# Kernel tuning notes

Hardware: AMD Instinct MI355X
Metric: run time of the kernel (lower is better)

The kernel has to match this reference:

```python
import jax, jax.numpy as jnp
import numpy as np

KERNEL = 25  # hard-coded moving-average kernel in the torch Model
HID = 128


def moving_avg(x):
    # x: [B, L, C]; edge-pad (KERNEL-1)//2 on each side along time, then mean over window
    p = (KERNEL - 1) // 2
    front = jnp.repeat(x[:, 0:1, :], p, axis=1)
    end = jnp.repeat(x[:, -1:, :], p, axis=1)
    xp = jnp.concatenate([front, x, end], axis=1)  # [B, L+2p, C]
    cs = jnp.cumsum(xp, axis=1)
    cs = jnp.concatenate([jnp.zeros_like(cs[:, :1, :]), cs], axis=1)
    return (cs[:, KERNEL:, :] - cs[:, :-KERNEL, :]) / KERNEL  # [B, L, C]


def memory_enhance(repres, memory):
    # repres: [N, 128], memory: [F, 128]
    attention = jax.nn.softmax(jnp.einsum('nd,fd->nf', repres, memory), axis=1)
    output = jnp.einsum('nf,fd->nd', attention, memory)
    return jnp.concatenate([output, repres], axis=1)  # [N, 256]


def setup_inputs() -> dict:
    key = jax.random.key(0)
    ks = jax.random.split(key, 12)
    B, L, C, P, M = 128, 720, 321, 336, 512
    s = lambda k, shape, fan: jax.random.normal(k, shape, jnp.float32) * (1.0 / np.sqrt(fan))
    return {
        'x': jax.random.normal(ks[0], (B, L, C), jnp.float32),
        'W_s1': s(ks[1], (HID, L), L), 'b_s1': jnp.zeros((HID,), jnp.float32),
        'W_s2': s(ks[2], (P, 2 * HID), 2 * HID), 'b_s2': jnp.zeros((P,), jnp.float32),
        'W_t1': s(ks[3], (HID, L), L), 'b_t1': jnp.zeros((HID,), jnp.float32),
        'W_t2': s(ks[4], (P, 2 * HID), 2 * HID), 'b_t2': jnp.zeros((P,), jnp.float32),
        'mem_S': s(ks[5], (M, HID), HID),
        'mem_T': s(ks[6], (M, HID), HID),
    }


def reference(x, W_s1, b_s1, W_s2, b_s2, W_t1, b_t1, W_t2, b_t2, mem_S, mem_T):
    B, L, C = x.shape
    trend = moving_avg(x)                 # [B, L, C]
    seasonal = x - trend
    seasonal = jnp.transpose(seasonal, (0, 2, 1))  # [B, C, L]
    trend = jnp.transpose(trend, (0, 2, 1))

    def branch(init, W1, b1, mem, W2, b2):
        r = jax.nn.sigmoid(jnp.einsum('bcl,hl->bch', init, W1) + b1)  # [B, C, 128]
        r = r.reshape(-1, HID)
        r = memory_enhance(r, mem)                                    # [N, 256]
        r = r.reshape(B, C, 2 * HID)
        return jnp.einsum('bcd,pd->bcp', r, W2) + b2                  # [B, C, P]

    seasonal_out = branch(seasonal, W_s1, b_s1, mem_S, W_s2, b_s2)
    trend_out = branch(trend, W_t1, b_t1, mem_T, W_t2, b_t2)
    return jnp.transpose(seasonal_out + trend_out, (0, 2, 1))  # [B, P, C]
```

## Files before the change

kernel.cpp:

```cpp
#include <hip/hip_runtime.h>
#include <math.h>

#define BB 128
#define LL 720
#define CC 321
#define HH 128
#define PP 336
#define MM 512
#define LPAD 736

typedef __attribute__((ext_vector_type(8))) short bf16x8;
typedef __attribute__((ext_vector_type(4))) float f32x4;

__device__ __forceinline__ short f2bf(float x) {
  unsigned u = __builtin_bit_cast(unsigned, x);
  u = (u + 0x7FFFu + ((u >> 16) & 1u)) >> 16;
  return (short)u;
}

__device__ __forceinline__ int packpos(int kw) {
  return ((kw & 15) >> 2) * 8 + (kw >> 4) * 4 + (kw & 3);
}

__global__ void weff_kernel(const float* __restrict__ Ws1,
                            const float* __restrict__ Wt1,
                            short* __restrict__ WsT,
                            short* __restrict__ WtT) {
  int idx = blockIdx.x * 256 + threadIdx.x;
  if (idx >= HH * LPAD) return;
  int j = idx % LPAD, h = idx / LPAD;
  int t = j >> 5, kw = j & 31;
  int dst = h * LPAD + t * 32 + packpos(kw);
  if (j >= LL) { WsT[dst] = 0; WtT[dst] = 0; return; }
  float ss = 0.f, st = 0.f;
  if (j == 0) {
    for (int l = 0; l <= 12; ++l) {
      float w = 13.f - (float)l;
      ss += w * Ws1[h * LL + l];
      st += w * Wt1[h * LL + l];
    }
  } else if (j == LL - 1) {
    for (int d = 0; d <= 12; ++d) {
      float w = 13.f - (float)d;
      ss += w * Ws1[h * LL + LL - 1 - d];
      st += w * Wt1[h * LL + LL - 1 - d];
    }
  } else {
    int lo = j - 12 < 0 ? 0 : j - 12;
    int hi = j + 12 > LL - 1 ? LL - 1 : j + 12;
    for (int l = lo; l <= hi; ++l) {
      ss += Ws1[h * LL + l];
      st += Wt1[h * LL + l];
    }
  }
  ss *= (1.f / 25.f);
  st *= (1.f / 25.f);
  WsT[dst] = f2bf(Ws1[h * LL + j] - ss);
  WtT[dst] = f2bf(st);
}

__global__ void memstage_kernel(const float* __restrict__ memS,
                                const float* __restrict__ memT,
                                short* __restrict__ stgS,
                                short* __restrict__ stgT) {
  int e = blockIdx.x * 256 + threadIdx.x;
  int br = e >> 14;
  int s = e & 16383;
  const float* src = br ? memT : memS;
  short* dst = br ? stgT : stgS;
  int tt = s >> 11;
  int c = s & 2047;
  int row = c >> 4, slot = c & 15;
  int sp = slot ^ (row & 7);
  int k = sp >> 2, lg = sp & 3;
  int ft = tt >> 1;
  short out[8];
  if ((tt & 1) == 0) {
    const float* r0 = src + (size_t)(ft * 128 + row) * 128 + k * 32 + lg * 4;
#pragma unroll
    for (int j = 0; j < 4; ++j) {
      out[j] = f2bf(r0[j]);
      out[j + 4] = f2bf(r0[16 + j]);
    }
  } else {
    int fbase = ft * 128 + k * 32 + lg * 4;
#pragma unroll
    for (int j = 0; j < 4; ++j) {
      out[j] = f2bf(src[(size_t)(fbase + j) * 128 + row]);
      out[j + 4] = f2bf(src[(size_t)(fbase + 16 + j) * 128 + row]);
    }
  }
  short4 a = make_short4(out[0], out[1], out[2], out[3]);
  short4 b = make_short4(out[4], out[5], out[6], out[7]);
  *(short4*)&dst[(size_t)s * 8] = a;
  *(short4*)&dst[(size_t)s * 8 + 4] = b;
}

__global__ void w2cvt_kernel(const float* __restrict__ Ws2,
                             const float* __restrict__ Wt2,
                             const float* __restrict__ bs2,
                             const float* __restrict__ bt2,
                             short* __restrict__ W2b, float* __restrict__ b2) {
  int i = blockIdx.x * 256 + threadIdx.x;
  if (i < PP) b2[i] = bs2[i] + bt2[i];
  if (i >= PP * 512) return;
  int p = i >> 9, k = i & 511;
  float v = (k < 256) ? Ws2[p * 256 + k] : Wt2[p * 256 + (k - 256)];
  W2b[p * 512 + (k >> 5) * 32 + packpos(k & 31)] = f2bf(v);
}

__global__ __launch_bounds__(256) void gemm1_mfma(
    const float* __restrict__ x,
    const short* __restrict__ WsT, const short* __restrict__ WtT,
    const float* __restrict__ bs1, const float* __restrict__ bt1,
    short* __restrict__ r2s, short* __restrict__ r2t) {
  __shared__ __align__(16) short wlds[2][2][128 * 40];
  __shared__ __align__(16) short xlds[2][64 * 40];
  int tid = threadIdx.x;
  int w = tid >> 6, l = tid & 63, lr = l & 15, lg = l >> 4;
  int ngrp = w >> 1, hhalf = w & 1, hb = hhalf * 64;
  int nb = blockIdx.x * 64;
  int cc0 = ngrp * 32 + lr, cc1 = cc0 + 16;
  int n0 = nb + cc0, n1 = nb + cc1;

  int rowA = tid >> 2, q = tid & 3;
  int rowB = rowA + 64;
  const short* gSA = WsT + rowA * LPAD + q * 8;
  const short* gSB = WsT + rowB * LPAD + q * 8;
  const short* gTA = WtT + rowA * LPAD + q * 8;
  const short* gTB = WtT + rowB * LPAD + q * 8;
  int dA = rowA * 40 + q * 8, dB = rowB * 40 + q * 8;

  int xcc = tid & 63, kg = tid >> 6;
  int xn = nb + xcc;
  int xb_ = xn / CC, xc_ = xn - xb_ * CC;
  const float* xptr = x + (size_t)xb_ * (LL * CC) + xc_;
  int dx0 = xcc * 40 + ((kg & 1) * 2 + 0) * 8 + (kg >> 1) * 4;
  int dx1 = xcc * 40 + ((kg & 1) * 2 + 1) * 8 + (kg >> 1) * 4;

  f32x4 acc[2][4][2];
#pragma unroll
  for (int br = 0; br < 2; ++br)
#pragma unroll
    for (int i = 0; i < 4; ++i)
#pragma unroll
      for (int rt = 0; rt < 2; ++rt) acc[br][i][rt] = (f32x4){0.f, 0.f, 0.f, 0.f};

  {
    int4 sA = *(const int4*)gSA;
    int4 sB = *(const int4*)gSB;
    int4 tA = *(const int4*)gTA;
    int4 tB = *(const int4*)gTB;
    *(int4*)&wlds[0][0][dA] = sA;
    *(int4*)&wlds[0][0][dB] = sB;
    *(int4*)&wlds[0][1][dA] = tA;
    *(int4*)&wlds[0][1][dB] = tB;
    float xf[8];
#pragma unroll
    for (int j = 0; j < 8; ++j) {
      int k = kg * 8 + j;
      xf[j] = xptr[(size_t)k * CC];
    }
    short4 s0 = make_short4(f2bf(xf[0]), f2bf(xf[1]), f2bf(xf[2]), f2bf(xf[3]));
    short4 s1 = make_short4(f2bf(xf[4]), f2bf(xf[5]), f2bf(xf[6]), f2bf(xf[7]));
    *(short4*)&xlds[0][dx0] = s0;
    *(short4*)&xlds[0][dx1] = s1;
  }
  __syncthreads();

  int cur = 0;
  for (int step = 0; step < 23; ++step) {
    int4 nSA = {0, 0, 0, 0}, nSB = nSA, nTA = nSA, nTB = nSA;
    float xf[8] = {0.f};
    if (step < 22) {
      int ko = (step + 1) * 32;
      nSA = *(const int4*)(gSA + ko);
      nSB = *(const int4*)(gSB + ko);
      nTA = *(const int4*)(gTA + ko);
      nTB = *(const int4*)(gTB + ko);
#pragma unroll
      for (int j = 0; j < 8; ++j) {
        int k = ko + kg * 8 + j;
        xf[j] = (k < LL) ? xptr[(size_t)k * CC] : 0.f;
      }
    }

    const short* xl = &xlds[cur][0];
    bf16x8 bx0 = *(const bf16x8*)&xl[cc0 * 40 + lg * 8];
    bf16x8 bx1 = *(const bf16x8*)&xl[cc1 * 40 + lg * 8];
    const short* tS = &wlds[cur][0][0];
    const short* tT = &wlds[cur][1][0];
#pragma unroll
    for (int ht = 0; ht < 4; ++ht) {
      int h = hb + ht * 16 + lr;
      bf16x8 aS = *(const bf16x8*)&tS[h * 40 + lg * 8];
      bf16x8 aT = *(const bf16x8*)&tT[h * 40 + lg * 8];
      acc[0][ht][0] =
          __builtin_amdgcn_mfma_f32_16x16x32_bf16(aS, bx0, acc[0][ht][0], 0, 0, 0);
      acc[0][ht][1] =
          __builtin_amdgcn_mfma_f32_16x16x32_bf16(aS, bx1, acc[0][ht][1], 0, 0, 0);
      acc[1][ht][0] =
          __builtin_amdgcn_mfma_f32_16x16x32_bf16(aT, bx0, acc[1][ht][0], 0, 0, 0);
      acc[1][ht][1] =
          __builtin_amdgcn_mfma_f32_16x16x32_bf16(aT, bx1, acc[1][ht][1], 0, 0, 0);
    }

    if (step < 22) {
      short* bS = &wlds[cur ^ 1][0][0];
      short* bT = &wlds[cur ^ 1][1][0];
      *(int4*)&bS[dA] = nSA;
      *(int4*)&bS[dB] = nSB;
      *(int4*)&bT[dA] = nTA;
      *(int4*)&bT[dB] = nTB;
      short4 s0 = make_short4(f2bf(xf[0]), f2bf(xf[1]), f2bf(xf[2]), f2bf(xf[3]));
      short4 s1 = make_short4(f2bf(xf[4]), f2bf(xf[5]), f2bf(xf[6]), f2bf(xf[7]));
      *(short4*)&xlds[cur ^ 1][dx0] = s0;
      *(short4*)&xlds[cur ^ 1][dx1] = s1;
    }
    __syncthreads();
    cur ^= 1;
  }

#pragma unroll
  for (int rt = 0; rt < 2; ++rt) {
    int n = rt ? n1 : n0;
    short* rowS = r2s + (size_t)n * 256 + 128;
    short* rowT = r2t + (size_t)n * 256 + 128;
#pragma unroll
    for (int ht = 0; ht < 4; ++ht) {
      int h = hb + ht * 16 + lg * 4;
      int hbase = hb + ht * 16;
      int dst = (hbase >> 5) * 32 + lg * 8 + ((hbase >> 4) & 1) * 4;
      float4 bS = *(const float4*)&bs1[h];
      float4 bT = *(const float4*)&bt1[h];
      const float* pbS = &bS.x;
      const float* pbT = &bT.x;
      short4 ss, st;
      short* ps = &ss.x;
      short* pt = &st.x;
#pragma unroll
      for (int j = 0; j < 4; ++j) {
        ps[j] = f2bf(1.f / (1.f + __expf(-(acc[0][ht][rt][j] + pbS[j]))));
        pt[j] = f2bf(1.f / (1.f + __expf(-(acc[1][ht][rt][j] + pbT[j]))));
      }
      *(short4*)&rowS[dst] = ss;
      *(short4*)&rowT[dst] = st;
    }
  }
}

__global__ __launch_bounds__(256) void memenh_mfma(
    const short* __restrict__ stgS, const short* __restrict__ stgT,
    short* __restrict__ r2s, short* __restrict__ r2t) {
  int br = blockIdx.y;
  const short* stg = br ? stgT : stgS;
  short* r2 = br ? r2t : r2s;

  __shared__ __align__(16) short buf[2][16384];
  int tid = threadIdx.x;
  int l = tid & 63, lr = l & 15, lg = l >> 4;
  int wbase = tid & 192;
  int n = blockIdx.x * 64 + (tid >> 6) * 16 + lr;

  bf16x8 brag[4];
  {
    const short* rb = r2 + (size_t)n * 256 + 128;
#pragma unroll
    for (int k = 0; k < 4; ++k)
      brag[k] = *(const bf16x8*)&rb[k * 32 + lg * 8];
  }

#define STAGE(t, bsel)                                                        \
  {                                                                           \
    const short* g = stg + (size_t)(t)*16384;                                 \
    _Pragma("unroll") for (int i = 0; i < 8; ++i) {                           \
      __builtin_amdgcn_global_load_lds(                                       \
          (const __attribute__((address_space(1))) unsigned int*)(            \
              g + (size_t)(i * 256 + tid) * 8),                               \
          (__attribute__((address_space(3))) unsigned int*)(                  \
              &buf[bsel][(i * 256 + wbase) * 8]),                             \
          16, 0, 0);                                                          \
    }                                                                         \
  }

  STAGE(0, 0);
  __syncthreads();

  f32x4 accO[8];
#pragma unroll
  for (int i = 0; i < 8; ++i) accO[i] = (f32x4){0.f, 0.f, 0.f, 0.f};
  bf16x8 pb[4];
  float ssum = 0.f;
  int cur = 0;

#pragma unroll
  for (int t = 0; t < 8; ++t) {
    if (t < 7) STAGE(t + 1, cur ^ 1);
    const short* tb = &buf[cur][0];
    if ((t & 1) == 0) {
      f32x4 sc[8];
#pragma unroll
      for (int ft16 = 0; ft16 < 8; ++ft16) {
        f32x4 a = {0.f, 0.f, 0.f, 0.f};
#pragma unroll
        for (int k = 0; k < 4; ++k) {
          int row = ft16 * 16 + lr;
          int slot = (4 * k + lg) ^ (row & 7);
          bf16x8 af = *(const bf16x8*)&tb[row * 128 + slot * 8];
          a = __builtin_amdgcn_mfma_f32_16x16x32_bf16(af, brag[k], a, 0, 0, 0);
        }
        sc[ft16] = a;
      }
#pragma unroll
      for (int i = 0; i < 8; ++i) {
        f32x4 v = sc[i];
#pragma unroll
        for (int j = 0; j < 4; ++j) {
          float e = __expf(v[j]);
          v[j] = e;
          ssum += e;
        }
        sc[i] = v;
      }
#pragma unroll
      for (int t4 = 0; t4 < 4; ++t4) {
        f32x4 e0 = sc[2 * t4], e1 = sc[2 * t4 + 1];
        bf16x8 f;
        f[0] = f2bf(e0[0]); f[1] = f2bf(e0[1]);
        f[2] = f2bf(e0[2]); f[3] = f2bf(e0[3]);
        f[4] = f2bf(e1[0]); f[5] = f2bf(e1[1]);
        f[6] = f2bf(e1[2]); f[7] = f2bf(e1[3]);
        pb[t4] = f;
      }
    } else {
#pragma unroll
      for (int dt = 0; dt < 8; ++dt) {
#pragma unroll
        for (int k = 0; k < 4; ++k) {
          int row = dt * 16 + lr;
          int slot = (4 * k + lg) ^ (row & 7);
          bf16x8 af = *(const bf16x8*)&tb[row * 128 + slot * 8];
          accO[dt] =
              __builtin_amdgcn_mfma_f32_16x16x32_bf16(af, pb[k], accO[dt], 0, 0, 0);
        }
      }
    }
    __syncthreads();
    cur ^= 1;
  }
#undef STAGE

  ssum += __shfl_xor(ssum, 16);
  ssum += __shfl_xor(ssum, 32);
  float inv = 1.f / ssum;
  short* rowO = r2 + (size_t)n * 256;
#pragma unroll
  for (int dt = 0; dt < 8; ++dt) {
    short4 o;
    o.x = f2bf(accO[dt][0] * inv);
    o.y = f2bf(accO[dt][1] * inv);
    o.z = f2bf(accO[dt][2] * inv);
    o.w = f2bf(accO[dt][3] * inv);
    *(short4*)&rowO[(dt >> 1) * 32 + lg * 8 + (dt & 1) * 4] = o;
  }
}

__global__ __launch_bounds__(512) void gemm2_mfma(
    const short* __restrict__ r2s, const short* __restrict__ r2t,
    const short* __restrict__ W2b,
    const float* __restrict__ b2,
    float* __restrict__ out) {
  __shared__ __align__(16) short w2lds[2][112 * 40];
  int tid = threadIdx.x;
  int w = tid >> 6, l = tid & 63, lr = l & 15, lg = l >> 4;
  int p0 = blockIdx.y * 112;
  int n = blockIdx.x * 128 + w * 16 + lr;
  int b = n / CC, c = n - b * CC;
  const short* rs = r2s + (size_t)n * 256;
  const short* rt = r2t + (size_t)n * 256;

  bool dostage = tid < 448;
  int row = tid >> 2, q = tid & 3;
  const short* gW = W2b + (size_t)(p0 + row) * 512 + q * 8;
  int doff = row * 40 + q * 8;

  f32x4 acc[7];
#pragma unroll
  for (int i = 0; i < 7; ++i) acc[i] = (f32x4){0.f, 0.f, 0.f, 0.f};

  if (dostage) *(int4*)&w2lds[0][doff] = *(const int4*)gW;
  __syncthreads();

  int cur = 0;
  for (int step = 0; step < 16; ++step) {
    int k0 = step * 32;
    const short* rrow = ((k0 < 256) ? rs : rt) + (k0 & 255);
    bf16x8 bfr = *(const bf16x8*)&rrow[lg * 8];
    int4 nxt = {0, 0, 0, 0};
    if (step < 15 && dostage) nxt = *(const int4*)(gW + (step + 1) * 32);
    const short* tw = &w2lds[cur][0];
#pragma unroll
    for (int pt = 0; pt < 7; ++pt) {
      bf16x8 a = *(const bf16x8*)&tw[(pt * 16 + lr) * 40 + lg * 8];
      acc[pt] = __builtin_amdgcn_mfma_f32_16x16x32_bf16(a, bfr, acc[pt], 0, 0, 0);
    }
    if (step < 15 && dostage) *(int4*)&w2lds[cur ^ 1][doff] = nxt;
    __syncthreads();
    cur ^= 1;
  }

  size_t obase = (size_t)b * ((size_t)PP * CC) + c;
#pragma unroll
  for (int pt = 0; pt < 7; ++pt) {
    int p = p0 + pt * 16 + lg * 4;
    float4 bias = *(const float4*)&b2[p];
    const float* pb = &bias.x;
#pragma unroll
    for (int j = 0; j < 4; ++j) {
      out[obase + (size_t)(p + j) * CC] = acc[pt][j] + pb[j];
    }
  }
}

extern "C" void kernel_launch(void* const* d_in, const int* in_sizes, int n_in,
                              void* d_out, int out_size, void* d_ws, size_t ws_size,
                              hipStream_t stream) {
  const float* x    = (const float*)d_in[0];
  const float* Ws1  = (const float*)d_in[1];
  const float* bs1  = (const float*)d_in[2];
  const float* Ws2  = (const float*)d_in[3];
  const float* bs2  = (const float*)d_in[4];
  const float* Wt1  = (const float*)d_in[5];
  const float* bt1  = (const float*)d_in[6];
  const float* Wt2  = (const float*)d_in[7];
  const float* bt2  = (const float*)d_in[8];
  const float* memS = (const float*)d_in[9];
  const float* memT = (const float*)d_in[10];
  float* out = (float*)d_out;

  const size_t N = (size_t)BB * CC;
  short* r2s  = (short*)d_ws;
  short* r2t  = r2s + N * 256;
  short* WsTb = r2t + N * 256;
  short* WtTb = WsTb + (size_t)HH * LPAD;
  short* stgS = WtTb + (size_t)HH * LPAD;
  short* stgT = stgS + (size_t)16384 * 8;
  short* W2b  = stgT + (size_t)16384 * 8;
  float* b2   = (float*)(W2b + (size_t)PP * 512);

  weff_kernel<<<(HH * LPAD) / 256, 256, 0, stream>>>(Ws1, Wt1, WsTb, WtTb);
  memstage_kernel<<<128, 256, 0, stream>>>(memS, memT, stgS, stgT);
  w2cvt_kernel<<<(PP * 512) / 256, 256, 0, stream>>>(Ws2, Wt2, bs2, bt2, W2b, b2);

  gemm1_mfma<<<642, 256, 0, stream>>>(x, WsTb, WtTb, bs1, bt1, r2s, r2t);

  dim3 g3(642, 2);
  memenh_mfma<<<g3, 256, 0, stream>>>(stgS, stgT, r2s, r2t);

  dim3 g2(321, 3);
  gemm2_mfma<<<g2, 512, 0, stream>>>(r2s, r2t, W2b, b2, out);
}
```

Before: 136.0 us.

## Stage gemm1 weights via swizzled pre-tiled image and direct global-to-LDS loads

The weight preprocessing kernel now writes a single pre-tiled, XOR-swizzled image of both branch weights in 64-wide K chunks. gemm1 fetches each chunk straight into LDS with global_load_lds instead of going through registers, and the x tile also uses a swizzled layout. The K step doubles from 32 to 64, cutting the number of barrier iterations from 23 to 12. The aim is fewer register round-trips, fewer LDS bank conflicts and less sync overhead, at the cost of larger LDS buffers, which may reduce occupancy, and extra zero padding in K (768 instead of 736).

```diff
diff --git a/kernel.cpp b/kernel.cpp
--- a/kernel.cpp
+++ b/kernel.cpp
@@ -7,7 +7,7 @@
 #define HH 128
 #define PP 336
 #define MM 512
-#define LPAD 736
+#define LPAD 768
 
 typedef __attribute__((ext_vector_type(8))) short bf16x8;
 typedef __attribute__((ext_vector_type(4))) float f32x4;
@@ -22,16 +22,28 @@
   return ((kw & 15) >> 2) * 8 + (kw >> 4) * 4 + (kw & 3);
 }
 
+__device__ __forceinline__ void gload_lds16(const short* g, short* l) {
+  __builtin_amdgcn_global_load_lds(
+      (const __attribute__((address_space(1))) unsigned int*)g,
+      (__attribute__((address_space(3))) unsigned int*)l, 16, 0, 0);
+}
+
 __global__ void weff_kernel(const float* __restrict__ Ws1,
                             const float* __restrict__ Wt1,
-                            short* __restrict__ WsT,
-                            short* __restrict__ WtT) {
+                            short* __restrict__ wimg) {
   int idx = blockIdx.x * 256 + threadIdx.x;
   if (idx >= HH * LPAD) return;
   int j = idx % LPAD, h = idx / LPAD;
-  int t = j >> 5, kw = j & 31;
-  int dst = h * LPAD + t * 32 + packpos(kw);
-  if (j >= LL) { WsT[dst] = 0; WtT[dst] = 0; return; }
+  int s = j >> 6, kw6 = j & 63, g = kw6 >> 5, kw = kw6 & 31;
+  int half = kw >> 4, lg = (kw >> 2) & 3, jj = kw & 3;
+  size_t base = ((size_t)(s * 128 + h)) * 128 + half * 4 + jj;
+  int slotS = g * 8 + ((0 + lg) ^ (h & 7));
+  int slotT = g * 8 + ((4 + lg) ^ (h & 7));
+  if (j >= LL) {
+    wimg[base + slotS * 8] = 0;
+    wimg[base + slotT * 8] = 0;
+    return;
+  }
   float ss = 0.f, st = 0.f;
   if (j == 0) {
     for (int l = 0; l <= 12; ++l) {
@@ -55,8 +67,8 @@
   }
   ss *= (1.f / 25.f);
   st *= (1.f / 25.f);
-  WsT[dst] = f2bf(Ws1[h * LL + j] - ss);
-  WtT[dst] = f2bf(st);
+  wimg[base + slotS * 8] = f2bf(Ws1[h * LL + j] - ss);
+  wimg[base + slotT * 8] = f2bf(st);
 }
 
 __global__ void memstage_kernel(const float* __restrict__ memS,
@@ -110,12 +122,11 @@
 }
 
 __global__ __launch_bounds__(256) void gemm1_mfma(
-    const float* __restrict__ x,
-    const short* __restrict__ WsT, const short* __restrict__ WtT,
+    const float* __restrict__ x, const short* __restrict__ wimg,
     const float* __restrict__ bs1, const float* __restrict__ bt1,
     short* __restrict__ r2s, short* __restrict__ r2t) {
-  __shared__ __align__(16) short wlds[2][2][128 * 40];
-  __shared__ __align__(16) short xlds[2][64 * 40];
+  __shared__ __align__(16) short wlds[2][16384];
+  __shared__ __align__(16) short xlds[2][4096];
   int tid = threadIdx.x;
   int w = tid >> 6, l = tid & 63, lr = l & 15, lg = l >> 4;
   int ngrp = w >> 1, hhalf = w & 1, hb = hhalf * 64;
@@ -123,20 +134,17 @@
   int cc0 = ngrp * 32 + lr, cc1 = cc0 + 16;
   int n0 = nb + cc0, n1 = nb + cc1;
 
-  int rowA = tid >> 2, q = tid & 3;
-  int rowB = rowA + 64;
-  const short* gSA = WsT + rowA * LPAD + q * 8;
-  const short* gSB = WsT + rowB * LPAD + q * 8;
-  const short* gTA = WtT + rowA * LPAD + q * 8;
-  const short* gTB = WtT + rowB * LPAD + q * 8;
-  int dA = rowA * 40 + q * 8, dB = rowB * 40 + q * 8;
-
-  int xcc = tid & 63, kg = tid >> 6;
+  int xcc = l;
+  int kg = w;
   int xn = nb + xcc;
   int xb_ = xn / CC, xc_ = xn - xb_ * CC;
   const float* xptr = x + (size_t)xb_ * (LL * CC) + xc_;
-  int dx0 = xcc * 40 + ((kg & 1) * 2 + 0) * 8 + (kg >> 1) * 4;
-  int dx1 = xcc * 40 + ((kg & 1) * 2 + 1) * 8 + (kg >> 1) * 4;
+  int xr = xcc >> 1, xodd = xcc & 1, xhalf = kg >> 1;
+  int lgA = (kg & 1) * 2;
+  int dxA = xr * 64 + (((xodd * 4 + lgA) ^ (xr & 7))) * 8 + xhalf * 4;
+  int dxB = xr * 64 + (((xodd * 4 + lgA + 1) ^ (xr & 7))) * 8 + xhalf * 4;
+
+  const short* wsrc0 = wimg + (size_t)(w * 512 + l * 8);
 
   f32x4 acc[2][4][2];
 #pragma unroll
@@ -147,75 +155,83 @@
       for (int rt = 0; rt < 2; ++rt) acc[br][i][rt] = (f32x4){0.f, 0.f, 0.f, 0.f};
 
   {
-    int4 sA = *(const int4*)gSA;
-    int4 sB = *(const int4*)gSB;
-    int4 tA = *(const int4*)gTA;
-    int4 tB = *(const int4*)gTB;
-    *(int4*)&wlds[0][0][dA] = sA;
-    *(int4*)&wlds[0][0][dB] = sB;
-    *(int4*)&wlds[0][1][dA] = tA;
-    *(int4*)&wlds[0][1][dB] = tB;
-    float xf[8];
-#pragma unroll
-    for (int j = 0; j < 8; ++j) {
-      int k = kg * 8 + j;
-      xf[j] = xptr[(size_t)k * CC];
-    }
-    short4 s0 = make_short4(f2bf(xf[0]), f2bf(xf[1]), f2bf(xf[2]), f2bf(xf[3]));
-    short4 s1 = make_short4(f2bf(xf[4]), f2bf(xf[5]), f2bf(xf[6]), f2bf(xf[7]));
-    *(short4*)&xlds[0][dx0] = s0;
-    *(short4*)&xlds[0][dx1] = s1;
+#pragma unroll
+    for (int i = 0; i < 8; ++i)
+      gload_lds16(wsrc0 + i * 2048, &wlds[0][i * 2048 + w * 512]);
+    float x0[16];
+#pragma unroll
+    for (int g = 0; g < 2; ++g)
+#pragma unroll
+      for (int m = 0; m < 8; ++m)
+        x0[g * 8 + m] = xptr[(size_t)(g * 32 + kg * 8 + m) * CC];
+#pragma unroll
+    for (int g = 0; g < 2; ++g) {
+      short4 a = make_short4(f2bf(x0[g * 8 + 0]), f2bf(x0[g * 8 + 1]),
+                             f2bf(x0[g * 8 + 2]), f2bf(x0[g * 8 + 3]));
+      short4 b = make_short4(f2bf(x0[g * 8 + 4]), f2bf(x0[g * 8 + 5]),
+                             f2bf(x0[g * 8 + 6]), f2bf(x0[g * 8 + 7]));
+      *(short4*)&xlds[0][g * 2048 + dxA] = a;
+      *(short4*)&xlds[0][g * 2048 + dxB] = b;
+    }
   }
   __syncthreads();
 
+  int r0 = cc0 >> 1, r1 = cc1 >> 1;
+  int sl0 = (((cc0 & 1) * 4 + lg) ^ (r0 & 7)) * 8;
+  int sl1 = (((cc1 & 1) * 4 + lg) ^ (r1 & 7)) * 8;
+
   int cur = 0;
-  for (int step = 0; step < 23; ++step) {
-    int4 nSA = {0, 0, 0, 0}, nSB = nSA, nTA = nSA, nTB = nSA;
-    float xf[8] = {0.f};
-    if (step < 22) {
-      int ko = (step + 1) * 32;
-      nSA = *(const int4*)(gSA + ko);
-      nSB = *(const int4*)(gSB + ko);
-      nTA = *(const int4*)(gTA + ko);
-      nTB = *(const int4*)(gTB + ko);
-#pragma unroll
-      for (int j = 0; j < 8; ++j) {
-        int k = ko + kg * 8 + j;
-        xf[j] = (k < LL) ? xptr[(size_t)k * CC] : 0.f;
-      }
-    }
-
-    const short* xl = &xlds[cur][0];
-    bf16x8 bx0 = *(const bf16x8*)&xl[cc0 * 40 + lg * 8];
-    bf16x8 bx1 = *(const bf16x8*)&xl[cc1 * 40 + lg * 8];
-    const short* tS = &wlds[cur][0][0];
-    const short* tT = &wlds[cur][1][0];
-#pragma unroll
-    for (int ht = 0; ht < 4; ++ht) {
-      int h = hb + ht * 16 + lr;
-      bf16x8 aS = *(const bf16x8*)&tS[h * 40 + lg * 8];
-      bf16x8 aT = *(const bf16x8*)&tT[h * 40 + lg * 8];
-      acc[0][ht][0] =
-          __builtin_amdgcn_mfma_f32_16x16x32_bf16(aS, bx0, acc[0][ht][0], 0, 0, 0);
-      acc[0][ht][1] =
-          __builtin_amdgcn_mfma_f32_16x16x32_bf16(aS, bx1, acc[0][ht][1], 0, 0, 0);
-      acc[1][ht][0] =
-          __builtin_amdgcn_mfma_f32_16x16x32_bf16(aT, bx0, acc[1][ht][0], 0, 0, 0);
-      acc[1][ht][1] =
-          __builtin_amdgcn_mfma_f32_16x16x32_bf16(aT, bx1, acc[1][ht][1], 0, 0, 0);
-    }
-
-    if (step < 22) {
-      short* bS = &wlds[cur ^ 1][0][0];
-      short* bT = &wlds[cur ^ 1][1][0];
-      *(int4*)&bS[dA] = nSA;
-      *(int4*)&bS[dB] = nSB;
-      *(int4*)&bT[dA] = nTA;
-      *(int4*)&bT[dB] = nTB;
-      short4 s0 = make_short4(f2bf(xf[0]), f2bf(xf[1]), f2bf(xf[2]), f2bf(xf[3]));
-      short4 s1 = make_short4(f2bf(xf[4]), f2bf(xf[5]), f2bf(xf[6]), f2bf(xf[7]));
-      *(short4*)&xlds[cur ^ 1][dx0] = s0;
-      *(short4*)&xlds[cur ^ 1][dx1] = s1;
+  for (int s = 0; s < 12; ++s) {
+    float xn_[16];
+    if (s < 11) {
+      int k0 = (s + 1) * 64;
+#pragma unroll
+      for (int g = 0; g < 2; ++g)
+#pragma unroll
+        for (int m = 0; m < 8; ++m) {
+          int k = k0 + g * 32 + kg * 8 + m;
+          xn_[g * 8 + m] = (k < LL) ? xptr[(size_t)k * CC] : 0.f;
+        }
+      const short* ws = wsrc0 + (size_t)(s + 1) * 16384;
+#pragma unroll
+      for (int i = 0; i < 8; ++i)
+        gload_lds16(ws + i * 2048, &wlds[cur ^ 1][i * 2048 + w * 512]);
+    }
+
+    const short* tw = &wlds[cur][0];
+    const short* tx = &xlds[cur][0];
+#pragma unroll
+    for (int g = 0; g < 2; ++g) {
+      bf16x8 bx0 = *(const bf16x8*)&tx[g * 2048 + r0 * 64 + sl0];
+      bf16x8 bx1 = *(const bf16x8*)&tx[g * 2048 + r1 * 64 + sl1];
+#pragma unroll
+      for (int ht = 0; ht < 4; ++ht) {
+        int h = hb + ht * 16 + lr;
+        bf16x8 aS = *(const bf16x8*)&tw[h * 128 + (g * 8 + (lg ^ (h & 7))) * 8];
+        bf16x8 aT =
+            *(const bf16x8*)&tw[h * 128 + (g * 8 + ((4 + lg) ^ (h & 7))) * 8];
+        acc[0][ht][0] =
+            __builtin_amdgcn_mfma_f32_16x16x32_bf16(aS, bx0, acc[0][ht][0], 0, 0, 0);
+        acc[0][ht][1] =
+            __builtin_amdgcn_mfma_f32_16x16x32_bf16(aS, bx1, acc[0][ht][1], 0, 0, 0);
+        acc[1][ht][0] =
+            __builtin_amdgcn_mfma_f32_16x16x32_bf16(aT, bx0, acc[1][ht][0], 0, 0, 0);
+        acc[1][ht][1] =
+            __builtin_amdgcn_mfma_f32_16x16x32_bf16(aT, bx1, acc[1][ht][1], 0, 0, 0);
+      }
+    }
+
+    if (s < 11) {
+      short* txn = &xlds[cur ^ 1][0];
+#pragma unroll
+      for (int g = 0; g < 2; ++g) {
+        short4 a = make_short4(f2bf(xn_[g * 8 + 0]), f2bf(xn_[g * 8 + 1]),
+                               f2bf(xn_[g * 8 + 2]), f2bf(xn_[g * 8 + 3]));
+        short4 b = make_short4(f2bf(xn_[g * 8 + 4]), f2bf(xn_[g * 8 + 5]),
+                               f2bf(xn_[g * 8 + 6]), f2bf(xn_[g * 8 + 7]));
+        *(short4*)&txn[g * 2048 + dxA] = a;
+        *(short4*)&txn[g * 2048 + dxB] = b;
+      }
     }
     __syncthreads();
     cur ^= 1;
@@ -274,12 +290,8 @@
   {                                                                           \
     const short* g = stg + (size_t)(t)*16384;                                 \
     _Pragma("unroll") for (int i = 0; i < 8; ++i) {                           \
-      __builtin_amdgcn_global_load_lds(                                       \
-          (const __attribute__((address_space(1))) unsigned int*)(            \
-              g + (size_t)(i * 256 + tid) * 8),                               \
-          (__attribute__((address_space(3))) unsigned int*)(                  \
-              &buf[bsel][(i * 256 + wbase) * 8]),                             \
-          16, 0, 0);                                                          \
+      gload_lds16(g + (size_t)(i * 256 + tid) * 8,                            \
+                  &buf[bsel][(i * 256 + wbase) * 8]);                         \
     }                                                                         \
   }
 
@@ -441,18 +453,17 @@
   const size_t N = (size_t)BB * CC;
   short* r2s  = (short*)d_ws;
   short* r2t  = r2s + N * 256;
-  short* WsTb = r2t + N * 256;
-  short* WtTb = WsTb + (size_t)HH * LPAD;
-  short* stgS = WtTb + (size_t)HH * LPAD;
+  short* wimg = r2t + N * 256;
+  short* stgS = wimg + (size_t)12 * 128 * 128;
   short* stgT = stgS + (size_t)16384 * 8;
   short* W2b  = stgT + (size_t)16384 * 8;
   float* b2   = (float*)(W2b + (size_t)PP * 512);
 
-  weff_kernel<<<(HH * LPAD) / 256, 256, 0, stream>>>(Ws1, Wt1, WsTb, WtTb);
+  weff_kernel<<<(HH * LPAD) / 256, 256, 0, stream>>>(Ws1, Wt1, wimg);
   memstage_kernel<<<128, 256, 0, stream>>>(memS, memT, stgS, stgT);
   w2cvt_kernel<<<(PP * 512) / 256, 256, 0, stream>>>(Ws2, Wt2, bs2, bt2, W2b, b2);
 
-  gemm1_mfma<<<642, 256, 0, stream>>>(x, WsTb, WtTb, bs1, bt1, r2s, r2t);
+  gemm1_mfma<<<642, 256, 0, stream>>>(x, wimg, bs1, bt1, r2s, r2t);
 
   dim3 g3(642, 2);
   memenh_mfma<<<g3, 256, 0, stream>>>(stgS, stgT, r2s, r2t);
```

New measurement: 142.6 us. 4.8% more time.
